# Kernel tuning notes

Measured on AMD Instinct MI355X. Metric: run time of the kernel, lower is better.

Reference implementation:

```python
import jax, jax.numpy as jnp
import numpy as np

# Dims: B batch, CK key dim, CV value dim, NOBJ objects, T memory frames, HxW feature map
B, CK, CV, NOBJ, T, H, W = 1, 64, 512, 2, 2, 64, 64


def setup_inputs() -> dict:
    key = jax.random.key(0)
    k1, k2, k3, k4, k5 = jax.random.split(key, 5)
    return {
        "query_key": jax.random.normal(k1, (B, CK, H, W), jnp.float32),
        "query_selection": jax.random.uniform(k2, (B, CK, H, W), jnp.float32),
        "memory_key": jax.random.normal(k3, (B, CK, T, H, W), jnp.float32),
        "memory_shrinkage": jax.random.uniform(k4, (B, 1, T, H, W), jnp.float32),
        "memory_value": jax.random.normal(k5, (B, NOBJ, CV, T, H, W), jnp.float32),
    }


def reference(query_key, query_selection, memory_key, memory_shrinkage, memory_value):
    b, nobj, cv = memory_value.shape[:3]
    ck = memory_key.shape[1]
    h, w = query_key.shape[-2:]
    hw = h * w
    mk = memory_key.reshape(b, ck, -1)            # (b, ck, N) with N = T*H*W
    ms = memory_shrinkage.reshape(b, -1)          # (b, N)
    qk = query_key.reshape(b, ck, hw)             # (b, ck, hw)
    qe = query_selection.reshape(b, ck, hw)       # (b, ck, hw)
    mv = memory_value.reshape(b, nobj * cv, -1)   # (b, nobj*cv, N)

    # Negative L2 similarity with selection weighting (XMem get_similarity)
    a_sq = jnp.einsum('bcn,bcp->bnp', mk * mk, qe)            # (b, N, hw)
    two_ab = 2.0 * jnp.einsum('bcn,bcp->bnp', mk, qk * qe)    # (b, N, hw)
    b_sq = jnp.sum(qe * qk * qk, axis=1, keepdims=True)       # (b, 1, hw)
    inv_sqrt_ck = np.float32(1.0 / np.sqrt(ck))
    sim = (two_ab - a_sq - b_sq) * ms[:, :, None] * inv_sqrt_ck

    # Softmax over memory slots (dim N), then weighted readout
    aff = jax.nn.softmax(sim, axis=1)                          # (b, N, hw)
    mem = jnp.einsum('bvn,bnp->bvp', mv, aff)                  # (b, nobj*cv, hw)
    return mem.reshape(b, nobj, cv, h, w)
```

## Files before the change

kernel.cpp:

```cpp
#include <hip/hip_runtime.h>
#include <stdint.h>

typedef unsigned short u16;
typedef __attribute__((ext_vector_type(4))) float f32x4;
typedef __attribute__((ext_vector_type(8))) __bf16 bf16x8;
typedef __attribute__((ext_vector_type(4))) unsigned int u32x4;

#define HWPX 4096
#define NMEM 8192
#define CKD  64
#define VROWS 1024

__device__ __forceinline__ u16 f2bf(float x) {
    union { float f; unsigned u; } v; v.f = x;
    unsigned r = v.u + 0x7FFFu + ((v.u >> 16) & 1u);
    return (u16)(r >> 16);
}

__device__ __forceinline__ void gld_lds16(const void* g, void* l) {
    __builtin_amdgcn_global_load_lds(
        (const __attribute__((address_space(1))) uint32_t*)g,
        (__attribute__((address_space(3))) uint32_t*)l, 16, 0, 0);
}


__global__ void prep_aux(const float* __restrict__ qk, const float* __restrict__ qe,
                         const float* __restrict__ mk, const float* __restrict__ mv,
                         u16* __restrict__ Qf, float* __restrict__ bsq,
                         u16* __restrict__ Kf, u16* __restrict__ mvb,
                         float* __restrict__ outz) {
    const int bx = blockIdx.x;
    const int tid = threadIdx.x;
    if (bx < 16) {
        int p = bx * 256 + tid;
        const int pt = p >> 7, wm = (p >> 6) & 1, mi = (p >> 4) & 3, l15 = p & 15;
        const size_t cb = ((((size_t)pt * 2 + 0) * 2 + wm) * 4 + mi) * 2;
        float acc = 0.f;
        #pragma unroll
        for (int cg = 0; cg < 8; ++cg) {
            const int kk = cg >> 2, quad = cg & 3;
            float kv[8], ev[8];
            #pragma unroll
            for (int j = 0; j < 8; ++j) {
                int c = cg * 8 + j;
                kv[j] = qk[c * HWPX + p];
                ev[j] = qe[c * HWPX + p];
                acc += ev[j] * kv[j] * kv[j];
            }
            unsigned w0[4], w1[4];
            #pragma unroll
            for (int jj = 0; jj < 4; ++jj) {
                w0[jj] = (unsigned)f2bf(kv[2*jj] * ev[2*jj]) |
                         ((unsigned)f2bf(kv[2*jj+1] * ev[2*jj+1]) << 16);
                w1[jj] = (unsigned)f2bf(ev[2*jj]) |
                         ((unsigned)f2bf(ev[2*jj+1]) << 16);
            }
            const size_t off = (size_t)quad * 128 + (size_t)l15 * 8;
            *(u32x4*)(Qf + (cb + kk) * 512 + off)      = (u32x4){w0[0], w0[1], w0[2], w0[3]};
            *(u32x4*)(Qf + (cb + 16 + kk) * 512 + off) = (u32x4){w1[0], w1[1], w1[2], w1[3]};
        }
        bsq[p] = acc;
        return;
    }
    if (bx < 48) {
        int n = (bx - 16) * 256 + tid;
        const int nt = n >> 7, wn = (n >> 6) & 1, ni = (n >> 4) & 3, l15 = n & 15;
        const size_t cb = ((((size_t)nt * 2 + 0) * 2 + wn) * 4 + ni) * 2;
        #pragma unroll
        for (int cg = 0; cg < 8; ++cg) {
            const int kk = cg >> 2, quad = cg & 3;
            float m[8];
            #pragma unroll
            for (int j = 0; j < 8; ++j)
                m[j] = mk[(cg * 8 + j) * NMEM + n];
            unsigned w0[4], w1[4];
            #pragma unroll
            for (int jj = 0; jj < 4; ++jj) {
                w0[jj] = (unsigned)f2bf(2.f * m[2*jj]) |
                         ((unsigned)f2bf(2.f * m[2*jj+1]) << 16);
                w1[jj] = (unsigned)f2bf(-m[2*jj] * m[2*jj]) |
                         ((unsigned)f2bf(-m[2*jj+1] * m[2*jj+1]) << 16);
            }
            const size_t off = (size_t)quad * 128 + (size_t)l15 * 8;
            *(u32x4*)(Kf + (cb + kk) * 512 + off)      = (u32x4){w0[0], w0[1], w0[2], w0[3]};
            *(u32x4*)(Kf + (cb + 16 + kk) * 512 + off) = (u32x4){w1[0], w1[1], w1[2], w1[3]};
        }
        return;
    }
    if (bx < 560) {
        const int blk = bx - 48;
        #pragma unroll 4
        for (int it = 0; it < 16; ++it) {
            int i = blk * 4096 + it * 256 + tid;
            float4 v = ((const float4*)mv)[i];
            u16 o0 = f2bf(v.x), o1 = f2bf(v.y), o2 = f2bf(v.z), o3 = f2bf(v.w);
            unsigned lo = (unsigned)o0 | ((unsigned)o1 << 16);
            unsigned hi = (unsigned)o2 | ((unsigned)o3 << 16);
            ((uint2*)mvb)[i] = make_uint2(lo, hi);
        }
        return;
    }
    {
        const int blk = bx - 560;
        #pragma unroll 4
        for (int it = 0; it < 16; ++it) {
            int i = blk * 4096 + it * 256 + tid;
            ((float4*)outz)[i] = make_float4(0.f, 0.f, 0.f, 0.f);
        }
    }
}

__launch_bounds__(256, 2)
__global__ void gemm1_tiles(const u16* __restrict__ Qf, const u16* __restrict__ Kf,
                            const float* __restrict__ bsq, const float* __restrict__ ms,
                            u16* __restrict__ Pt, float* __restrict__ dpart) {
    __shared__ __align__(16) u16 smem[17408];

    const int tile = blockIdx.x;
    const int pb = tile & 31;
    const int nb = tile >> 5;
    const int p0 = pb * 128;
    const int n0 = nb * 128;

    const int tid  = threadIdx.x;
    const int l    = tid & 63;
    const int w    = tid >> 6;
    const int quad = l >> 4;
    const int l15  = l & 15;
    const int wm = w >> 1, wn = w & 1;

    f32x4 acc[4][4] = {};

    #pragma unroll
    for (int h = 0; h < 2; ++h) {
        bf16x8 a[4][2], b[4][2];
        const u16* qbase = Qf + ((((size_t)pb * 2 + h) * 2 + wm) * 4096) + (size_t)l * 8;
        const u16* kbase = Kf + ((((size_t)nb * 2 + h) * 2 + wn) * 4096) + (size_t)l * 8;
        #pragma unroll
        for (int mi = 0; mi < 4; ++mi) {
            a[mi][0] = *(const bf16x8*)(qbase + mi * 1024);
            a[mi][1] = *(const bf16x8*)(qbase + mi * 1024 + 512);
        }
        #pragma unroll
        for (int ni = 0; ni < 4; ++ni) {
            b[ni][0] = *(const bf16x8*)(kbase + ni * 1024);
            b[ni][1] = *(const bf16x8*)(kbase + ni * 1024 + 512);
        }
        #pragma unroll
        for (int kk = 0; kk < 2; ++kk)
            #pragma unroll
            for (int mi = 0; mi < 4; ++mi)
                #pragma unroll
                for (int ni = 0; ni < 4; ++ni)
                    acc[mi][ni] = __builtin_amdgcn_mfma_f32_16x16x32_bf16(a[mi][kk], b[ni][kk], acc[mi][ni], 0, 0, 0);
    }

    float msv[4];
    #pragma unroll
    for (int ni = 0; ni < 4; ++ni)
        msv[ni] = ms[n0 + wn * 64 + ni * 16 + l15] * 0.125f;
    float bsv[4][4];
    #pragma unroll
    for (int mi = 0; mi < 4; ++mi)
        #pragma unroll
        for (int r = 0; r < 4; ++r)
            bsv[mi][r] = bsq[p0 + wm * 64 + mi * 16 + quad * 4 + r];

    u16* Ps = smem;
    float rowsum[4][4] = {};
    #pragma unroll
    for (int mi = 0; mi < 4; ++mi) {
        #pragma unroll
        for (int ni = 0; ni < 4; ++ni) {
            f32x4 v = acc[mi][ni];
            int col = wn * 64 + ni * 16 + l15;
            #pragma unroll
            for (int r = 0; r < 4; ++r) {
                int rowl = wm * 64 + mi * 16 + quad * 4 + r;
                float pv = __expf((v[r] - bsv[mi][r]) * msv[ni]);
                rowsum[mi][r] += pv;
                Ps[rowl * 136 + col] = f2bf(pv);
            }
        }
    }
    #pragma unroll
    for (int mi = 0; mi < 4; ++mi)
        #pragma unroll
        for (int r = 0; r < 4; ++r) {
            float s = rowsum[mi][r];
            s += __shfl_xor(s, 1);
            s += __shfl_xor(s, 2);
            s += __shfl_xor(s, 4);
            s += __shfl_xor(s, 8);
            rowsum[mi][r] = s;
        }
    {
        float myv = 0.f;
        #pragma unroll
        for (int mi = 0; mi < 4; ++mi)
            #pragma unroll
            for (int r = 0; r < 4; ++r)
                if (l15 == mi * 4 + r) myv = rowsum[mi][r];
        int slice = nb * 2 + wn;
        dpart[(size_t)slice * HWPX + p0 + wm * 64 + (l15 >> 2) * 16 + quad * 4 + (l15 & 3)] = myv;
    }
    __syncthreads();

    {
        const size_t dstBase = (size_t)pb * 1048576 + (size_t)nb * 16384;
        #pragma unroll
        for (int it = 0; it < 8; ++it) {
            const int combo = it * 4 + w;
            const int kt  = combo >> 4;
            const int wnq = (combo >> 3) & 1;
            const int niq = (combo >> 1) & 3;
            const int kkq = combo & 1;
            const u32x4* src = (const u32x4*)(Ps + (wnq * 64 + niq * 16 + l15) * 136
                                                 + kt * 64 + kkq * 32 + quad * 8);
            u32x4* dst = (u32x4*)(Pt + dstBase + kt * 8192 + wnq * 4096
                                     + niq * 1024 + kkq * 512 + l * 8);
            *dst = *src;
        }
    }
}

__global__ void denom_kernel(const float* __restrict__ dpart, float* __restrict__ dinvg) {
    const int p = blockIdx.x * 256 + threadIdx.x;
    float s = 0.f;
    #pragma unroll 8
    for (int sl = 0; sl < 128; ++sl)
        s += dpart[(size_t)sl * HWPX + p];
    dinvg[p] = 1.0f / s;
}

__launch_bounds__(256, 4)
__global__ void gemm2_kernel(const u16* __restrict__ Ab, const u16* __restrict__ Btf,
                             const float* __restrict__ dinvg, float* __restrict__ outacc) {
    __shared__ __align__(16) u16 As[128 * 64];

    const int tid  = threadIdx.x;
    const int l    = tid & 63;
    const int w    = tid >> 6;
    const int quad = l >> 4;
    const int l15  = l & 15;
    const int wm = w >> 1, wn = w & 1;

    const int vb = blockIdx.x;
    const int pb = blockIdx.y;
    const int kz = blockIdx.z;
    const int v0 = vb * 128;
    const int p0 = pb * 128;
    const int kbeg = kz * (NMEM / 8);

    const int rsub = tid >> 3;
    const int csw  = (tid & 7) ^ (rsub & 7);

    const u16* bbase = Btf + (size_t)pb * 1048576 + (size_t)wn * 4096 + (size_t)l * 8;

    f32x4 acc[4][4] = {};

    for (int t = 0; t < 16; ++t) {
        const int k0 = kbeg + t * 64;
        const int kt = k0 >> 6;
        __syncthreads();
        #pragma unroll
        for (int rnd = 0; rnd < 4; ++rnd)
            gld_lds16(Ab + (size_t)(v0 + rnd * 32 + rsub) * NMEM + k0 + csw * 8,
                      As + rnd * 2048 + w * 512);
        bf16x8 b[4][2];
        {
            const u16* bk = bbase + (size_t)kt * 8192;
            #pragma unroll
            for (int ni = 0; ni < 4; ++ni) {
                b[ni][0] = *(const bf16x8*)(bk + ni * 1024);
                b[ni][1] = *(const bf16x8*)(bk + ni * 1024 + 512);
            }
        }
        __syncthreads();
        #pragma unroll
        for (int kk = 0; kk < 2; ++kk) {
            bf16x8 a[4];
            #pragma unroll
            for (int mi = 0; mi < 4; ++mi) {
                int row = wm * 64 + mi * 16 + l15;
                a[mi] = *(const bf16x8*)(As + row * 64 + (((kk * 4 + quad) ^ (l15 & 7)) << 3));
            }
            #pragma unroll
            for (int mi = 0; mi < 4; ++mi)
                #pragma unroll
                for (int ni = 0; ni < 4; ++ni)
                    acc[mi][ni] = __builtin_amdgcn_mfma_f32_16x16x32_bf16(a[mi], b[ni][kk], acc[mi][ni], 0, 0, 0);
        }
    }

    float dinv[4];
    #pragma unroll
    for (int ni = 0; ni < 4; ++ni)
        dinv[ni] = dinvg[p0 + wn * 64 + ni * 16 + l15];

    #pragma unroll
    for (int mi = 0; mi < 4; ++mi) {
        #pragma unroll
        for (int ni = 0; ni < 4; ++ni) {
            int col = p0 + wn * 64 + ni * 16 + l15;
            f32x4 v = acc[mi][ni];
            #pragma unroll
            for (int r = 0; r < 4; ++r) {
                int row = v0 + wm * 64 + mi * 16 + quad * 4 + r;
                atomicAdd(&outacc[(size_t)row * HWPX + col], v[r] * dinv[ni]);
            }
        }
    }
}

extern "C" void kernel_launch(void* const* d_in, const int* in_sizes, int n_in,
                              void* d_out, int out_size, void* d_ws, size_t ws_size,
                              hipStream_t stream) {
    const float* qk = (const float*)d_in[0];
    const float* qe = (const float*)d_in[1];
    const float* mk = (const float*)d_in[2];
    const float* ms = (const float*)d_in[3];
    const float* mv = (const float*)d_in[4];
    float* out = (float*)d_out;

    char* ws = (char*)d_ws;
    u16*   Pt    = (u16*)ws;
    u16*   mvb   = (u16*)(ws + ((size_t)64 << 20));
    u16*   Kf    = (u16*)(ws + ((size_t)80 << 20));
    u16*   Qf    = (u16*)(ws + ((size_t)82 << 20));
    float* bsq   = (float*)(ws + ((size_t)83 << 20));
    float* dpart = (float*)(ws + ((size_t)83 << 20) + 65536);
    float* dinvg = (float*)(ws + ((size_t)83 << 20) + 65536 + (2 << 20));

    prep_aux<<<816, 256, 0, stream>>>(qk, qe, mk, mv, Qf, bsq, Kf, mvb, out);

    gemm1_tiles<<<2048, 256, 0, stream>>>(Qf, Kf, bsq, ms, Pt, dpart);

    denom_kernel<<<16, 256, 0, stream>>>(dpart, dinvg);

    dim3 g2(8, 32, 8);
    gemm2_kernel<<<g2, 256, 0, stream>>>(mvb, Pt, dinvg, out);
}
```

Before: 267.8 us.

## Drop split-K atomics in readout GEMM, add triple-buffered LDS pipeline

The readout GEMM no longer splits K across 8 blocks with atomicAdd into a zeroed output. Each block now covers the full K range over a 64x128 output tile and writes results with plain stores, so the zero-fill pass in the prep kernel is removed. The K loop uses a three-buffer LDS ring with explicit waitcnt, barriers and raised priority around the MFMAs, and a swizzled 1D grid that groups blocks for reuse. There are fewer, longer blocks (512), and each block does more serial K iterations.

After: 219.1 us. 1.22x faster.

```diff
diff --git a/kernel.cpp b/kernel.cpp
--- a/kernel.cpp
+++ b/kernel.cpp
@@ -27,8 +27,7 @@
 __global__ void prep_aux(const float* __restrict__ qk, const float* __restrict__ qe,
                          const float* __restrict__ mk, const float* __restrict__ mv,
                          u16* __restrict__ Qf, float* __restrict__ bsq,
-                         u16* __restrict__ Kf, u16* __restrict__ mvb,
-                         float* __restrict__ outz) {
+                         u16* __restrict__ Kf, u16* __restrict__ mvb) {
     const int bx = blockIdx.x;
     const int tid = threadIdx.x;
     if (bx < 16) {
@@ -87,7 +86,7 @@
         }
         return;
     }
-    if (bx < 560) {
+    {
         const int blk = bx - 48;
         #pragma unroll 4
         for (int it = 0; it < 16; ++it) {
@@ -97,15 +96,6 @@
             unsigned lo = (unsigned)o0 | ((unsigned)o1 << 16);
             unsigned hi = (unsigned)o2 | ((unsigned)o3 << 16);
             ((uint2*)mvb)[i] = make_uint2(lo, hi);
-        }
-        return;
-    }
-    {
-        const int blk = bx - 560;
-        #pragma unroll 4
-        for (int it = 0; it < 16; ++it) {
-            int i = blk * 4096 + it * 256 + tid;
-            ((float4*)outz)[i] = make_float4(0.f, 0.f, 0.f, 0.f);
         }
     }
 }
@@ -236,7 +226,7 @@
 __launch_bounds__(256, 4)
 __global__ void gemm2_kernel(const u16* __restrict__ Ab, const u16* __restrict__ Btf,
                              const float* __restrict__ dinvg, float* __restrict__ outacc) {
-    __shared__ __align__(16) u16 As[128 * 64];
+    __shared__ __align__(16) u16 As3[3 * 4096];
 
     const int tid  = threadIdx.x;
     const int l    = tid & 63;
@@ -245,53 +235,74 @@
     const int l15  = l & 15;
     const int wm = w >> 1, wn = w & 1;
 
-    const int vb = blockIdx.x;
-    const int pb = blockIdx.y;
-    const int kz = blockIdx.z;
-    const int v0 = vb * 128;
+    const int lin = blockIdx.x;
+    const int pb  = (lin & 7) | (((lin >> 7) & 3) << 3);
+    const int vb  = (lin >> 3) & 15;
+    const int v0 = vb * 64;
     const int p0 = pb * 128;
-    const int kbeg = kz * (NMEM / 8);
+    const int NT = NMEM / 64;
 
     const int rsub = tid >> 3;
     const int csw  = (tid & 7) ^ (rsub & 7);
 
     const u16* bbase = Btf + (size_t)pb * 1048576 + (size_t)wn * 4096 + (size_t)l * 8;
 
-    f32x4 acc[4][4] = {};
-
-    for (int t = 0; t < 16; ++t) {
-        const int k0 = kbeg + t * 64;
-        const int kt = k0 >> 6;
-        __syncthreads();
-        #pragma unroll
-        for (int rnd = 0; rnd < 4; ++rnd)
-            gld_lds16(Ab + (size_t)(v0 + rnd * 32 + rsub) * NMEM + k0 + csw * 8,
-                      As + rnd * 2048 + w * 512);
+    u16* pR = As3;
+    u16* pN = As3 + 4096;
+    u16* pS = As3 + 8192;
+
+    #define STAGE_A(k0g, dst)                                                    \
+        { _Pragma("unroll")                                                      \
+          for (int rnd = 0; rnd < 2; ++rnd)                                      \
+              gld_lds16(Ab + (size_t)(v0 + rnd * 32 + rsub) * NMEM + (k0g) + csw * 8, \
+                        (dst) + rnd * 2048 + w * 512); }
+
+    f32x4 acc[2][4] = {};
+
+    STAGE_A(0, pR)
+    STAGE_A(64, pN)
+    asm volatile("s_waitcnt vmcnt(2)" ::: "memory");
+    __builtin_amdgcn_s_barrier();
+    __builtin_amdgcn_sched_barrier(0);
+
+    for (int t = 0; t < NT; ++t) {
+        const bool st = (t + 2 < NT);
         bf16x8 b[4][2];
-        {
-            const u16* bk = bbase + (size_t)kt * 8192;
-            #pragma unroll
-            for (int ni = 0; ni < 4; ++ni) {
-                b[ni][0] = *(const bf16x8*)(bk + ni * 1024);
-                b[ni][1] = *(const bf16x8*)(bk + ni * 1024 + 512);
-            }
-        }
-        __syncthreads();
-        #pragma unroll
-        for (int kk = 0; kk < 2; ++kk) {
-            bf16x8 a[4];
-            #pragma unroll
-            for (int mi = 0; mi < 4; ++mi) {
-                int row = wm * 64 + mi * 16 + l15;
-                a[mi] = *(const bf16x8*)(As + row * 64 + (((kk * 4 + quad) ^ (l15 & 7)) << 3));
-            }
-            #pragma unroll
-            for (int mi = 0; mi < 4; ++mi)
+        const u16* bk = bbase + (size_t)t * 8192;
+        #pragma unroll
+        for (int ni = 0; ni < 4; ++ni) {
+            b[ni][0] = *(const bf16x8*)(bk + ni * 1024);
+            b[ni][1] = *(const bf16x8*)(bk + ni * 1024 + 512);
+        }
+        __builtin_amdgcn_sched_barrier(0);
+        if (st) STAGE_A((t + 2) * 64, pS)
+        bf16x8 a[2][2];
+        #pragma unroll
+        for (int kk = 0; kk < 2; ++kk)
+            #pragma unroll
+            for (int mi = 0; mi < 2; ++mi) {
+                int row = wm * 32 + mi * 16 + l15;
+                a[mi][kk] = *(const bf16x8*)(pR + row * 64 + (((kk * 4 + quad) ^ (l15 & 7)) << 3));
+            }
+        __builtin_amdgcn_sched_barrier(0);
+        if (st) { asm volatile("s_waitcnt vmcnt(2)" ::: "memory"); }
+        else    { asm volatile("s_waitcnt vmcnt(0)" ::: "memory"); }
+        asm volatile("s_waitcnt lgkmcnt(0)" ::: "memory");
+        __builtin_amdgcn_sched_barrier(0);
+        __builtin_amdgcn_s_setprio(1);
+        #pragma unroll
+        for (int kk = 0; kk < 2; ++kk)
+            #pragma unroll
+            for (int mi = 0; mi < 2; ++mi)
                 #pragma unroll
                 for (int ni = 0; ni < 4; ++ni)
-                    acc[mi][ni] = __builtin_amdgcn_mfma_f32_16x16x32_bf16(a[mi], b[ni][kk], acc[mi][ni], 0, 0, 0);
-        }
-    }
+                    acc[mi][ni] = __builtin_amdgcn_mfma_f32_16x16x32_bf16(a[mi][kk], b[ni][kk], acc[mi][ni], 0, 0, 0);
+        __builtin_amdgcn_s_setprio(0);
+        __builtin_amdgcn_s_barrier();
+        __builtin_amdgcn_sched_barrier(0);
+        u16* tmp = pR; pR = pN; pN = pS; pS = tmp;
+    }
+    #undef STAGE_A
 
     float dinv[4];
     #pragma unroll
@@ -299,15 +310,15 @@
         dinv[ni] = dinvg[p0 + wn * 64 + ni * 16 + l15];
 
     #pragma unroll
-    for (int mi = 0; mi < 4; ++mi) {
+    for (int mi = 0; mi < 2; ++mi) {
         #pragma unroll
         for (int ni = 0; ni < 4; ++ni) {
             int col = p0 + wn * 64 + ni * 16 + l15;
             f32x4 v = acc[mi][ni];
             #pragma unroll
             for (int r = 0; r < 4; ++r) {
-                int row = v0 + wm * 64 + mi * 16 + quad * 4 + r;
-                atomicAdd(&outacc[(size_t)row * HWPX + col], v[r] * dinv[ni]);
+                int row = v0 + wm * 32 + mi * 16 + quad * 4 + r;
+                outacc[(size_t)row * HWPX + col] = v[r] * dinv[ni];
             }
         }
     }
@@ -332,12 +343,11 @@
     float* dpart = (float*)(ws + ((size_t)83 << 20) + 65536);
     float* dinvg = (float*)(ws + ((size_t)83 << 20) + 65536 + (2 << 20));
 
-    prep_aux<<<816, 256, 0, stream>>>(qk, qe, mk, mv, Qf, bsq, Kf, mvb, out);
+    prep_aux<<<560, 256, 0, stream>>>(qk, qe, mk, mv, Qf, bsq, Kf, mvb);
 
     gemm1_tiles<<<2048, 256, 0, stream>>>(Qf, Kf, bsq, ms, Pt, dpart);
 
     denom_kernel<<<16, 256, 0, stream>>>(dpart, dinvg);
 
-    dim3 g2(8, 32, 8);
-    gemm2_kernel<<<g2, 256, 0, stream>>>(mvb, Pt, dinvg, out);
-}
+    gemm2_kernel<<<512, 256, 0, stream>>>(mvb, Pt, dinvg, out);
+}
```

## Pre-swizzle value matrix into MFMA fragment layout and register-pipeline gemm2

Applied to the files above, without the earlier changes.

The mv bf16 conversion now writes directly into an MFMA-fragment-ordered layout, and the P tile layout is changed to 256-column blocks. This lets gemm2 load both A and B fragments straight from global memory into registers with no LDS or syncthreads. gemm2 now uses 512-thread blocks with a 128x256 output tile and a K split of 2 instead of 8, which cuts atomic traffic. Its loop double-buffers register loads with explicit waitcnt and setprio. In exchange the prep step has far fewer threads doing strided conversion, and register pressure rises, which may lower occupancy.

After: 264.4 us. No clear change (-1.3%).

```diff
diff --git a/kernel.cpp b/kernel.cpp
--- a/kernel.cpp
+++ b/kernel.cpp
@@ -17,17 +17,11 @@
     return (u16)(r >> 16);
 }
 
-__device__ __forceinline__ void gld_lds16(const void* g, void* l) {
-    __builtin_amdgcn_global_load_lds(
-        (const __attribute__((address_space(1))) uint32_t*)g,
-        (__attribute__((address_space(3))) uint32_t*)l, 16, 0, 0);
-}
-
 
 __global__ void prep_aux(const float* __restrict__ qk, const float* __restrict__ qe,
                          const float* __restrict__ mk, const float* __restrict__ mv,
                          u16* __restrict__ Qf, float* __restrict__ bsq,
-                         u16* __restrict__ Kf, u16* __restrict__ mvb,
+                         u16* __restrict__ Kf, u16* __restrict__ Avf,
                          float* __restrict__ outz) {
     const int bx = blockIdx.x;
     const int tid = threadIdx.x;
@@ -87,21 +81,28 @@
         }
         return;
     }
-    if (bx < 560) {
-        const int blk = bx - 48;
-        #pragma unroll 4
-        for (int it = 0; it < 16; ++it) {
-            int i = blk * 4096 + it * 256 + tid;
-            float4 v = ((const float4*)mv)[i];
-            u16 o0 = f2bf(v.x), o1 = f2bf(v.y), o2 = f2bf(v.z), o3 = f2bf(v.w);
-            unsigned lo = (unsigned)o0 | ((unsigned)o1 << 16);
-            unsigned hi = (unsigned)o2 | ((unsigned)o3 << 16);
-            ((uint2*)mvb)[i] = make_uint2(lo, hi);
+    if (bx < 80) {
+        const int idx = (bx - 48) * 256 + tid;
+        const int v = idx >> 3, og = idx & 7;
+        const int vt = v >> 7, wm = (v >> 6) & 1, mi = (v >> 4) & 3, l15 = v & 15;
+        const float* src = mv + (size_t)v * NMEM + (size_t)og * 1024;
+        u16* dbase = Avf + (size_t)vt * 1048576 + wm * 4096 + mi * 1024 + l15 * 8;
+        for (int i = 0; i < 128; ++i) {
+            const int oct = og * 128 + i;
+            float4 f0 = *(const float4*)(src + i * 8);
+            float4 f1 = *(const float4*)(src + i * 8 + 4);
+            unsigned w0 = (unsigned)f2bf(f0.x) | ((unsigned)f2bf(f0.y) << 16);
+            unsigned w1 = (unsigned)f2bf(f0.z) | ((unsigned)f2bf(f0.w) << 16);
+            unsigned w2 = (unsigned)f2bf(f1.x) | ((unsigned)f2bf(f1.y) << 16);
+            unsigned w3 = (unsigned)f2bf(f1.z) | ((unsigned)f2bf(f1.w) << 16);
+            const int kt = oct >> 3, kk = (oct >> 2) & 1, quad = oct & 3;
+            *(u32x4*)(dbase + (size_t)kt * 8192 + kk * 512 + quad * 128) =
+                (u32x4){w0, w1, w2, w3};
         }
         return;
     }
     {
-        const int blk = bx - 560;
+        const int blk = bx - 80;
         #pragma unroll 4
         for (int it = 0; it < 16; ++it) {
             int i = blk * 4096 + it * 256 + tid;
@@ -207,7 +208,7 @@
     __syncthreads();
 
     {
-        const size_t dstBase = (size_t)pb * 1048576 + (size_t)nb * 16384;
+        const size_t dstBase = (size_t)(pb >> 1) * 2097152 + (size_t)(pb & 1) * 2 * 4096;
         #pragma unroll
         for (int it = 0; it < 8; ++it) {
             const int combo = it * 4 + w;
@@ -217,8 +218,8 @@
             const int kkq = combo & 1;
             const u32x4* src = (const u32x4*)(Ps + (wnq * 64 + niq * 16 + l15) * 136
                                                  + kt * 64 + kkq * 32 + quad * 8);
-            u32x4* dst = (u32x4*)(Pt + dstBase + kt * 8192 + wnq * 4096
-                                     + niq * 1024 + kkq * 512 + l * 8);
+            u32x4* dst = (u32x4*)(Pt + dstBase + (size_t)(nb * 2 + kt) * 16384
+                                     + wnq * 4096 + niq * 1024 + kkq * 512 + l * 8);
             *dst = *src;
         }
     }
@@ -233,65 +234,81 @@
     dinvg[p] = 1.0f / s;
 }
 
-__launch_bounds__(256, 4)
-__global__ void gemm2_kernel(const u16* __restrict__ Ab, const u16* __restrict__ Btf,
+__launch_bounds__(512, 2)
+__global__ void gemm2_kernel(const u16* __restrict__ Avf, const u16* __restrict__ Btf,
                              const float* __restrict__ dinvg, float* __restrict__ outacc) {
-    __shared__ __align__(16) u16 As[128 * 64];
-
     const int tid  = threadIdx.x;
     const int l    = tid & 63;
     const int w    = tid >> 6;
     const int quad = l >> 4;
     const int l15  = l & 15;
-    const int wm = w >> 1, wn = w & 1;
-
-    const int vb = blockIdx.x;
-    const int pb = blockIdx.y;
-    const int kz = blockIdx.z;
+    const int wm = w >> 2;
+    const int wn = w & 3;
+
+    const int pB = blockIdx.x | ((blockIdx.z & 1) << 3);
+    const int kz = blockIdx.y;
+    const int vb = blockIdx.z >> 1;
     const int v0 = vb * 128;
-    const int p0 = pb * 128;
-    const int kbeg = kz * (NMEM / 8);
-
-    const int rsub = tid >> 3;
-    const int csw  = (tid & 7) ^ (rsub & 7);
-
-    const u16* bbase = Btf + (size_t)pb * 1048576 + (size_t)wn * 4096 + (size_t)l * 8;
+    const int p0 = pB * 256;
+    const int NT = 64;
+
+    const u16* abase = Avf + (size_t)vb * 1048576 + (size_t)wm * 4096 + (size_t)l * 8
+                           + (size_t)(kz * 64) * 8192;
+    const u16* bbase = Btf + (size_t)pB * 2097152 + (size_t)wn * 4096 + (size_t)l * 8
+                           + (size_t)(kz * 64) * 16384;
+
+    #define LOADA(dst, t_)                                                       \
+        { const u16* ak = abase + (size_t)(t_) * 8192;                           \
+          _Pragma("unroll")                                                      \
+          for (int mi = 0; mi < 4; ++mi) {                                       \
+              dst[mi][0] = *(const bf16x8*)(ak + mi * 1024);                     \
+              dst[mi][1] = *(const bf16x8*)(ak + mi * 1024 + 512);               \
+          } }
+    #define LOADB(dst, t_)                                                       \
+        { const u16* bk = bbase + (size_t)(t_) * 16384;                          \
+          _Pragma("unroll")                                                      \
+          for (int ni = 0; ni < 4; ++ni) {                                       \
+              dst[ni][0] = *(const bf16x8*)(bk + ni * 1024);                     \
+              dst[ni][1] = *(const bf16x8*)(bk + ni * 1024 + 512);               \
+          } }
+    #define DOMFMA(A_, B_)                                                       \
+        { _Pragma("unroll")                                                      \
+          for (int kk = 0; kk < 2; ++kk)                                         \
+              _Pragma("unroll")                                                  \
+              for (int mi = 0; mi < 4; ++mi)                                     \
+                  _Pragma("unroll")                                              \
+                  for (int ni = 0; ni < 4; ++ni)                                 \
+                      acc[mi][ni] = __builtin_amdgcn_mfma_f32_16x16x32_bf16(     \
+                          A_[mi][kk], B_[ni][kk], acc[mi][ni], 0, 0, 0); }
 
     f32x4 acc[4][4] = {};
-
-    for (int t = 0; t < 16; ++t) {
-        const int k0 = kbeg + t * 64;
-        const int kt = k0 >> 6;
-        __syncthreads();
-        #pragma unroll
-        for (int rnd = 0; rnd < 4; ++rnd)
-            gld_lds16(Ab + (size_t)(v0 + rnd * 32 + rsub) * NMEM + k0 + csw * 8,
-                      As + rnd * 2048 + w * 512);
-        bf16x8 b[4][2];
-        {
-            const u16* bk = bbase + (size_t)kt * 8192;
-            #pragma unroll
-            for (int ni = 0; ni < 4; ++ni) {
-                b[ni][0] = *(const bf16x8*)(bk + ni * 1024);
-                b[ni][1] = *(const bf16x8*)(bk + ni * 1024 + 512);
-            }
-        }
-        __syncthreads();
-        #pragma unroll
-        for (int kk = 0; kk < 2; ++kk) {
-            bf16x8 a[4];
-            #pragma unroll
-            for (int mi = 0; mi < 4; ++mi) {
-                int row = wm * 64 + mi * 16 + l15;
-                a[mi] = *(const bf16x8*)(As + row * 64 + (((kk * 4 + quad) ^ (l15 & 7)) << 3));
-            }
-            #pragma unroll
-            for (int mi = 0; mi < 4; ++mi)
-                #pragma unroll
-                for (int ni = 0; ni < 4; ++ni)
-                    acc[mi][ni] = __builtin_amdgcn_mfma_f32_16x16x32_bf16(a[mi], b[ni][kk], acc[mi][ni], 0, 0, 0);
-        }
-    }
+    bf16x8 aC[4][2], bC[4][2], aN[4][2], bN[4][2];
+
+    LOADA(aC, 0) LOADB(bC, 0)
+    for (int t = 0; t < NT; t += 2) {
+        LOADA(aN, t + 1) LOADB(bN, t + 1)
+        __builtin_amdgcn_sched_barrier(0);
+        asm volatile("s_waitcnt vmcnt(16)" ::: "memory");
+        __builtin_amdgcn_sched_barrier(0);
+        __builtin_amdgcn_s_setprio(1);
+        DOMFMA(aC, bC)
+        __builtin_amdgcn_s_setprio(0);
+        if (t + 2 < NT) {
+            LOADA(aC, t + 2) LOADB(bC, t + 2)
+            __builtin_amdgcn_sched_barrier(0);
+            asm volatile("s_waitcnt vmcnt(16)" ::: "memory");
+        } else {
+            __builtin_amdgcn_sched_barrier(0);
+            asm volatile("s_waitcnt vmcnt(0)" ::: "memory");
+        }
+        __builtin_amdgcn_sched_barrier(0);
+        __builtin_amdgcn_s_setprio(1);
+        DOMFMA(aN, bN)
+        __builtin_amdgcn_s_setprio(0);
+    }
+    #undef LOADA
+    #undef LOADB
+    #undef DOMFMA
 
     float dinv[4];
     #pragma unroll
@@ -325,19 +342,19 @@
 
     char* ws = (char*)d_ws;
     u16*   Pt    = (u16*)ws;
-    u16*   mvb   = (u16*)(ws + ((size_t)64 << 20));
+    u16*   Avf   = (u16*)(ws + ((size_t)64 << 20));
     u16*   Kf    = (u16*)(ws + ((size_t)80 << 20));
     u16*   Qf    = (u16*)(ws + ((size_t)82 << 20));
     float* bsq   = (float*)(ws + ((size_t)83 << 20));
     float* dpart = (float*)(ws + ((size_t)83 << 20) + 65536);
     float* dinvg = (float*)(ws + ((size_t)83 << 20) + 65536 + (2 << 20));
 
-    prep_aux<<<816, 256, 0, stream>>>(qk, qe, mk, mv, Qf, bsq, Kf, mvb, out);
+    prep_aux<<<336, 256, 0, stream>>>(qk, qe, mk, mv, Qf, bsq, Kf, Avf, out);
 
     gemm1_tiles<<<2048, 256, 0, stream>>>(Qf, Kf, bsq, ms, Pt, dpart);
 
     denom_kernel<<<16, 256, 0, stream>>>(dpart, dinvg);
 
-    dim3 g2(8, 32, 8);
-    gemm2_kernel<<<g2, 256, 0, stream>>>(mvb, Pt, dinvg, out);
-}
+    dim3 g2(8, 2, 16);
+    gemm2_kernel<<<g2, 512, 0, stream>>>(Avf, Pt, dinvg, out);
+}
```
